# Kernel tuning notes

Hardware: AMD Instinct MI355X
Metric: run time of the kernel (lower is better)

The kernel has to match this reference:

```python
import jax, jax.numpy as jnp
import numpy as np

B, N, D, K, L, H, DFF = 2048, 64, 256, 32, 2, 8, 1024
TEMP = 10.0
EPS = 1e-10


def _ln(x, g, b):
    m = jnp.mean(x, -1, keepdims=True)
    v = jnp.mean((x - m) ** 2, -1, keepdims=True)
    return (x - m) * jax.lax.rsqrt(v + 1e-5) * g + b


def _mha(x, Wqkv, bqkv, Wo, bo):
    b, n, d = x.shape
    dh = d // H
    qkv = x @ Wqkv.T + bqkv                      # [b,n,3d]
    q, k, v = jnp.split(qkv, 3, axis=-1)
    q = q.reshape(b, n, H, dh)
    k = k.reshape(b, n, H, dh)
    v = v.reshape(b, n, H, dh)
    att = jnp.einsum('bqhd,bkhd->bhqk', q, k) / np.float32(np.sqrt(dh))
    att = jax.nn.softmax(att, axis=-1)
    o = jnp.einsum('bhqk,bkhd->bqhd', att, v).reshape(b, n, d)
    return o @ Wo.T + bo


def _encoder(x, Wqkv, bqkv, Wo, bo, ln1_g, ln1_b, ln2_g, ln2_b, W1, b1, W2, b2):
    # torch TransformerEncoder, norm_first=False (post-LN), dropout=0
    for l in range(L):
        x = _ln(x + _mha(x, Wqkv[l], bqkv[l], Wo[l], bo[l]), ln1_g[l], ln1_b[l])
        h = jax.nn.relu(x @ W1[l].T + b1[l]) @ W2[l].T + b2[l]
        x = _ln(x + h, ln2_g[l], ln2_b[l])
    return x


def _cluster_probs_from_emb(emb, mus):
    # ||x - tanh(mu)||^2 via expansion to avoid the [B,N,K,D] intermediate
    mt = jnp.tanh(mus)                                       # [K,D]
    d2 = (jnp.sum(emb ** 2, -1)[..., None]
          - 2.0 * jnp.einsum('bnd,kd->bnk', emb, mt)
          + jnp.sum(mt ** 2, -1))                            # [B,N,K]
    e = jnp.exp(-d2 / TEMP)
    return e / jnp.sum(e, -1, keepdims=True)


def _forward(input_series, init_logits, transition_logits,
             Wqkv, bqkv, Wo, bo, ln1_g, ln1_b, ln2_g, ln2_b,
             W1, b1, W2, b2, mus):
    prob_pi = jax.nn.softmax(init_logits, axis=0)            # [K]
    prob_A = jax.nn.softmax(transition_logits, axis=1)       # [K,K]
    emb_all = _encoder(input_series, Wqkv, bqkv, Wo, bo,
                       ln1_g, ln1_b, ln2_g, ln2_b, W1, b1, W2, b2)
    logits_all = _cluster_probs_from_emb(emb_all, mus)       # [B,N,K]

    log_emit = jnp.log(logits_all + EPS)                     # [B,N,K]
    lt0 = jax.nn.softmax(jnp.log(prob_pi + EPS)[None, :] + log_emit[:, 0], axis=1)

    def step(lt, le):
        lt = jax.nn.softmax(jnp.log(lt @ prob_A + EPS) + le, axis=1)
        return lt, lt

    _, rest = jax.lax.scan(step, lt0, jnp.swapaxes(log_emit[:, 1:], 0, 1))
    cluster_probs = jnp.concatenate([lt0[:, None], jnp.swapaxes(rest, 0, 1)], axis=1)
    entropy_loss = -jnp.mean(jnp.sum(cluster_probs * jnp.log(cluster_probs + EPS), -1))
    return cluster_probs, emb_all, prob_pi, prob_A, entropy_loss


def setup_inputs() -> dict:
    key = jax.random.key(0)
    ks = jax.random.split(key, 10)
    s = jnp.float32(0.02)
    return {
        'input_series': jax.random.normal(ks[0], (B, N, D), jnp.float32),
        'init_logits': jax.random.normal(ks[1], (K,), jnp.float32),
        'transition_logits': jax.random.normal(ks[2], (K, K), jnp.float32),
        'Wqkv': jax.random.normal(ks[3], (L, 3 * D, D), jnp.float32) * s,
        'bqkv': jnp.zeros((L, 3 * D), jnp.float32),
        'Wo': jax.random.normal(ks[4], (L, D, D), jnp.float32) * s,
        'bo': jnp.zeros((L, D), jnp.float32),
        'ln1_g': jnp.ones((L, D), jnp.float32),
        'ln1_b': jnp.zeros((L, D), jnp.float32),
        'ln2_g': jnp.ones((L, D), jnp.float32),
        'ln2_b': jnp.zeros((L, D), jnp.float32),
        'W1': jax.random.normal(ks[5], (L, DFF, D), jnp.float32) * s,
        'b1': jnp.zeros((L, DFF), jnp.float32),
        'W2': jax.random.normal(ks[6], (L, D, DFF), jnp.float32) * s,
        'b2': jnp.zeros((L, D), jnp.float32),
        'mus': jax.random.normal(ks[7], (K, D), jnp.float32),
    }


def reference(input_series, init_logits, transition_logits, Wqkv, bqkv, Wo, bo,
              ln1_g, ln1_b, ln2_g, ln2_b, W1, b1, W2, b2, mus):
    return _forward(input_series, init_logits, transition_logits, Wqkv, bqkv,
                    Wo, bo, ln1_g, ln1_b, ln2_g, ln2_b, W1, b1, W2, b2, mus)
```

## Files before the change

kernel.cpp:

```cpp
#include <hip/hip_runtime.h>

#define BB   2048
#define NNX  64
#define DD   256
#define KKC  32
#define LLN  2
#define HHN  8
#define DHH  32
#define DFFN 1024
#define BNT  (BB*NNX)

typedef short s16x8 __attribute__((ext_vector_type(8)));
typedef float f32x4 __attribute__((ext_vector_type(4)));

#define GLOAD_LDS16(gp, lp) __builtin_amdgcn_global_load_lds( \
    (const __attribute__((address_space(1))) void*)(gp),      \
    (__attribute__((address_space(3))) void*)(lp), 16, 0, 0)

#define WAITVM4() asm volatile("s_waitcnt vmcnt(4)" ::: "memory")
#define WAITVM0() asm volatile("s_waitcnt vmcnt(0)" ::: "memory")
#define WAITLGKM0() do { asm volatile("s_waitcnt lgkmcnt(0)" ::: "memory"); \
                         __builtin_amdgcn_sched_barrier(0); } while (0)
#define SBAR() __builtin_amdgcn_s_barrier()

__device__ __forceinline__ unsigned short f2bf(float f) {
  unsigned int u = __float_as_uint(f);
  u += 0x7fffu + ((u >> 16) & 1u);
  return (unsigned short)(u >> 16);
}
__device__ __forceinline__ float bf2f(unsigned short u) {
  return __uint_as_float(((unsigned int)u) << 16);
}

__global__ __launch_bounds__(256) void cvt_kernel(const float4* __restrict__ src,
                                                  ushort4* __restrict__ dst, int n4) {
  int i = blockIdx.x * 256 + threadIdx.x;
  int st = gridDim.x * 256;
  for (; i < n4; i += st) {
    float4 v = src[i];
    ushort4 o;
    o.x = f2bf(v.x); o.y = f2bf(v.y); o.z = f2bf(v.z); o.w = f2bf(v.w);
    dst[i] = o;
  }
}

__global__ __launch_bounds__(256) void cvtw_kernel(const float4* __restrict__ wq, ushort4* __restrict__ dq,
                                                   const float4* __restrict__ wo, ushort4* __restrict__ dov,
                                                   const float4* __restrict__ w1, ushort4* __restrict__ d1,
                                                   const float4* __restrict__ w2, ushort4* __restrict__ d2) {
  const int n0 = 98304, n1 = 32768, n2 = 131072, n3 = 131072;
  int i = blockIdx.x * 256 + threadIdx.x;
  int st = gridDim.x * 256;
  for (; i < n0 + n1 + n2 + n3; i += st) {
    const float4* s; ushort4* d; int j = i;
    if (j < n0) { s = wq; d = dq; }
    else if ((j -= n0) < n1) { s = wo; d = dov; }
    else if ((j -= n1) < n2) { s = w1; d = d1; }
    else { j -= n2; s = w2; d = d2; }
    float4 v = s[j];
    ushort4 o;
    o.x = f2bf(v.x); o.y = f2bf(v.y); o.z = f2bf(v.z); o.w = f2bf(v.w);
    d[j] = o;
  }
}

__global__ void mt_kernel(const float* __restrict__ mus, float* __restrict__ mtT,
                          float* __restrict__ mtn) {
  int k = threadIdx.x;
  if (k < 32) {
    float acc = 0.f;
    for (int d = 0; d < 256; d++) {
      float t = tanhf(mus[k * 256 + d]);
      mtT[d * 32 + k] = t;
      acc += t * t;
    }
    mtn[k] = acc;
  }
}

__global__ void piA_kernel(const float* __restrict__ il, const float* __restrict__ tl,
                           float* __restrict__ d_pi, float* __restrict__ d_A,
                           float* __restrict__ d_ent) {
  int lane = threadIdx.x;
  if (lane == 0) *d_ent = 0.f;
  if (lane < 32) {
    float v = il[lane];
    float mx = v;
    #pragma unroll
    for (int off = 16; off; off >>= 1) mx = fmaxf(mx, __shfl_xor(mx, off, 32));
    float e = expf(v - mx), sm = e;
    #pragma unroll
    for (int off = 16; off; off >>= 1) sm += __shfl_xor(sm, off, 32);
    d_pi[lane] = e / sm;
    for (int r = 0; r < 32; r++) {
      float a = tl[r * 32 + lane];
      float m2 = a;
      #pragma unroll
      for (int off = 16; off; off >>= 1) m2 = fmaxf(m2, __shfl_xor(m2, off, 32));
      float e2 = expf(a - m2), s2 = e2;
      #pragma unroll
      for (int off = 16; off; off >>= 1) s2 += __shfl_xor(s2, off, 32);
      d_A[r * 32 + lane] = e2 / s2;
    }
  }
}

template <int EPI>
__global__ __launch_bounds__(256, 4) void gemm_nt(const unsigned short* __restrict__ A,
                                                  const unsigned short* __restrict__ Bw,
                                                  const float* __restrict__ bias,
                                                  unsigned short* __restrict__ outp,
                                                  int N, int K, int nx) {
  __shared__ unsigned short lds[16384];
  const int t = threadIdx.x;
  const int bid = blockIdx.x, nwg = gridDim.x;
  const int wg = (bid & 7) * (nwg >> 3) + (bid >> 3);
  const int m0 = (wg / nx) << 7;
  const int n0 = (wg % nx) << 7;
  const int lane = t & 63, w = t >> 6;
  const int wm = w >> 1, wn = w & 1;
  const int lr = lane & 15, lk = lane >> 4;

  const int r0 = t >> 2, sg = t & 3;
  const int s0 = sg ^ ((r0 >> 1) & 3);
  const int r1 = r0 + 64;
  const int s1 = sg ^ ((r1 >> 1) & 3);
  const int aoff0 = (m0 + r0) * K + s0 * 8;
  const int aoff1 = (m0 + r1) * K + s1 * 8;
  const int boff0 = (n0 + r0) * K + s0 * 8;
  const int boff1 = (n0 + r1) * K + s1 * 8;

#define STAGE(buf, k0) do {                                    \
    char* la = (char*)lds + (buf) * 16384;                     \
    GLOAD_LDS16(A + aoff0 + (k0), la + t * 16);                \
    GLOAD_LDS16(A + aoff1 + (k0), la + 4096 + t * 16);         \
    GLOAD_LDS16(Bw + boff0 + (k0), la + 8192 + t * 16);        \
    GLOAD_LDS16(Bw + boff1 + (k0), la + 12288 + t * 16);       \
  } while (0)

  f32x4 acc[4][4];
  #pragma unroll
  for (int i = 0; i < 4; i++)
    #pragma unroll
    for (int j = 0; j < 4; j++) acc[i][j] = (f32x4)(0.f);

  const int ra = wm * 64 + lr, rb = wn * 64 + lr;
  const int sla = lk ^ ((ra >> 1) & 3), slb = lk ^ ((rb >> 1) & 3);

  const int NT = K >> 5;
  STAGE(0, 0);
  STAGE(1, 32);
  WAITVM4();
  SBAR();

  int c = 0;
  for (int kt = 0; kt < NT; kt++) {
    s16x8 af[4], bf[4];
    {
      const unsigned short* ua = lds + c * 8192;
      const unsigned short* ub = ua + 4096;
      #pragma unroll
      for (int mf = 0; mf < 4; mf++)
        af[mf] = *(const s16x8*)&ua[(ra + mf * 16) * 32 + sla * 8];
      #pragma unroll
      for (int nf = 0; nf < 4; nf++)
        bf[nf] = *(const s16x8*)&ub[(rb + nf * 16) * 32 + slb * 8];
    }
    __builtin_amdgcn_s_setprio(1);
    #pragma unroll
    for (int mf = 0; mf < 4; mf++)
      #pragma unroll
      for (int nf = 0; nf < 4; nf++)
        acc[mf][nf] = __builtin_amdgcn_mfma_f32_16x16x32_bf16(af[mf], bf[nf], acc[mf][nf], 0, 0, 0);
    __builtin_amdgcn_s_setprio(0);
    SBAR();
    if (kt < NT - 2) {
      STAGE(c, (kt + 2) << 5);
      WAITVM4();
    } else if (kt == NT - 2) {
      WAITVM0();
    }
    SBAR();
    c ^= 1;
  }
#undef STAGE

  #pragma unroll
  for (int nf = 0; nf < 4; nf++) {
    int col = n0 + wn * 64 + nf * 16 + lr;
    float bv = bias[col];
    #pragma unroll
    for (int mf = 0; mf < 4; mf++)
      #pragma unroll
      for (int r = 0; r < 4; r++) {
        int row = m0 + wm * 64 + mf * 16 + lk * 4 + r;
        float v = acc[mf][nf][r] + bv;
        if (EPI == 1) v = fmaxf(v, 0.f);
        outp[(size_t)row * N + col] = f2bf(v);
      }
  }
}

template <bool WR32>
__global__ __launch_bounds__(512) void gemm_ln(const unsigned short* __restrict__ A,
                                               const unsigned short* __restrict__ Bw,
                                               const float* __restrict__ bias,
                                               const unsigned short* __restrict__ res,
                                               const float* __restrict__ g,
                                               const float* __restrict__ bta,
                                               unsigned short* __restrict__ xb,
                                               float* __restrict__ x32,
                                               int K) {
  __shared__ unsigned short As[128 * 64];
  __shared__ unsigned short Bs[256 * 64];
  __shared__ float stats[2][128][4];
  const int t = threadIdx.x;
  const int nwg = gridDim.x;
  const int bid = blockIdx.x;
  const int wg = (bid & 7) * (nwg >> 3) + (bid >> 3);
  const int m0 = wg << 7;

  const int lane = t & 63, w = t >> 6;
  const int wm = w >> 2, wn = w & 3;
  const int lr = lane & 15, lk = lane >> 4;

  size_t aoff[2], boff[4];
  #pragma unroll
  for (int p = 0; p < 2; p++) {
    int u = p * 512 + t;
    int row = u >> 3, sp = u & 7;
    int seg = sp ^ (((row >> 2) & 1) << 1);
    aoff[p] = (size_t)(m0 + row) * K + seg * 8;
  }
  #pragma unroll
  for (int p = 0; p < 4; p++) {
    int u = p * 512 + t;
    int row = u >> 3, sp = u & 7;
    int seg = sp ^ (((row >> 2) & 1) << 1);
    boff[p] = (size_t)row * K + seg * 8;
  }

  f32x4 acc[4][4];
  #pragma unroll
  for (int i = 0; i < 4; i++)
    #pragma unroll
    for (int j = 0; j < 4; j++) acc[i][j] = (f32x4)(0.f);

  for (int k0 = 0; k0 < K; k0 += 64) {
    #pragma unroll
    for (int p = 0; p < 2; p++)
      GLOAD_LDS16(A + aoff[p] + k0, (char*)As + (p * 512 + t) * 16);
    #pragma unroll
    for (int p = 0; p < 4; p++)
      GLOAD_LDS16(Bw + boff[p] + k0, (char*)Bs + (p * 512 + t) * 16);
    __syncthreads();
    #pragma unroll
    for (int z = 0; z < 2; z++) {
      s16x8 af[4], bfr[4];
      #pragma unroll
      for (int mf = 0; mf < 4; mf++) {
        int row = wm * 64 + mf * 16 + lr;
        int cc = (z * 4 + lk) ^ (((row >> 2) & 1) << 1);
        af[mf] = *(const s16x8*)&As[row * 64 + cc * 8];
      }
      #pragma unroll
      for (int nf = 0; nf < 4; nf++) {
        int row = wn * 64 + nf * 16 + lr;
        int cc = (z * 4 + lk) ^ (((row >> 2) & 1) << 1);
        bfr[nf] = *(const s16x8*)&Bs[row * 64 + cc * 8];
      }
      #pragma unroll
      for (int mf = 0; mf < 4; mf++)
        #pragma unroll
        for (int nf = 0; nf < 4; nf++)
          acc[mf][nf] = __builtin_amdgcn_mfma_f32_16x16x32_bf16(af[mf], bfr[nf], acc[mf][nf], 0, 0, 0);
    }
    __syncthreads();
  }

  float bv[4];
  #pragma unroll
  for (int nf = 0; nf < 4; nf++) bv[nf] = bias[wn * 64 + nf * 16 + lr];

  #pragma unroll
  for (int mf = 0; mf < 4; mf++) {
    #pragma unroll
    for (int r = 0; r < 4; r++) {
      int grow = m0 + wm * 64 + mf * 16 + lk * 4 + r;
      float s = 0.f, q = 0.f;
      #pragma unroll
      for (int nf = 0; nf < 4; nf++) {
        int col = wn * 64 + nf * 16 + lr;
        float v = acc[mf][nf][r] + bv[nf] + bf2f(res[(size_t)grow * 256 + col]);
        acc[mf][nf][r] = v;
        s += v; q += v * v;
      }
      #pragma unroll
      for (int off = 1; off < 16; off <<= 1) { s += __shfl_xor(s, off); q += __shfl_xor(q, off); }
      if (lr == 0) {
        int lrow = wm * 64 + mf * 16 + lk * 4 + r;
        stats[0][lrow][wn] = s;
        stats[1][lrow][wn] = q;
      }
    }
  }
  __syncthreads();

  float gv[4], bbv[4];
  #pragma unroll
  for (int nf = 0; nf < 4; nf++) {
    int col = wn * 64 + nf * 16 + lr;
    gv[nf] = g[col]; bbv[nf] = bta[col];
  }
  #pragma unroll
  for (int mf = 0; mf < 4; mf++) {
    #pragma unroll
    for (int r = 0; r < 4; r++) {
      int lrow = wm * 64 + mf * 16 + lk * 4 + r;
      int grow = m0 + lrow;
      float s4 = stats[0][lrow][0] + stats[0][lrow][1] + stats[0][lrow][2] + stats[0][lrow][3];
      float q4 = stats[1][lrow][0] + stats[1][lrow][1] + stats[1][lrow][2] + stats[1][lrow][3];
      float mean = s4 * (1.f / 256.f);
      float var = q4 * (1.f / 256.f) - mean * mean;
      float rs = rsqrtf(var + 1e-5f);
      #pragma unroll
      for (int nf = 0; nf < 4; nf++) {
        int col = wn * 64 + nf * 16 + lr;
        float val = (acc[mf][nf][r] - mean) * rs * gv[nf] + bbv[nf];
        xb[(size_t)grow * 256 + col] = f2bf(val);
        if (WR32) x32[(size_t)grow * 256 + col] = val;
      }
    }
  }
}

__global__ __launch_bounds__(64) void attn_kernel(const unsigned short* __restrict__ qkv,
                                                  unsigned short* __restrict__ ob) {
  __shared__ unsigned short al[6784];
  unsigned short* qs = al;
  unsigned short* ks = al + 2048;
  unsigned short* vs = al + 4608;
  unsigned short* vt = al;
  unsigned short* ps = al + 2176;
  const int bh = blockIdx.x;
  const int b = bh >> 3, h = bh & 7;
  const int lane = threadIdx.x;
  const int lr = lane & 15, lk = lane >> 4;

  #pragma unroll
  for (int p = 0; p < 4; p++) {
    int u = lane + p * 64;
    int row = u >> 2, seg = u & 3;
    size_t gb = (size_t)(b * 64 + row) * 768 + h * 32 + seg * 8;
    GLOAD_LDS16(qkv + gb, (char*)al + u * 16);
    GLOAD_LDS16(qkv + gb + 256, (char*)al + 4096 + u * 16);
    GLOAD_LDS16(qkv + gb + 512, (char*)al + 9216 + u * 16);
  }
  __syncthreads();

  s16x8 aq[4], bk[4], vchunk[4];
  #pragma unroll
  for (int mi = 0; mi < 4; mi++) aq[mi] = *(const s16x8*)&qs[(mi * 16 + lr) * 32 + lk * 8];
  #pragma unroll
  for (int nj = 0; nj < 4; nj++) bk[nj] = *(const s16x8*)&ks[(nj * 16 + lr) * 32 + lk * 8];
  const int vrow = lane >> 2, vcs = (lane & 3) * 8;
  #pragma unroll
  for (int q = 0; q < 4; q++)
    vchunk[q] = *(const s16x8*)&vs[(q * 16 + vrow) * 32 + vcs];
  WAITLGKM0();

  #pragma unroll
  for (int q = 0; q < 4; q++)
    #pragma unroll
    for (int j = 0; j < 8; j++)
      vt[(vcs + j) * 68 + q * 16 + vrow] = (unsigned short)vchunk[q][j];

  f32x4 s[4][4];
  #pragma unroll
  for (int i = 0; i < 4; i++)
    #pragma unroll
    for (int j = 0; j < 4; j++) s[i][j] = (f32x4)(0.f);
  #pragma unroll
  for (int mi = 0; mi < 4; mi++)
    #pragma unroll
    for (int nj = 0; nj < 4; nj++)
      s[mi][nj] = __builtin_amdgcn_mfma_f32_16x16x32_bf16(aq[mi], bk[nj], s[mi][nj], 0, 0, 0);

  const float scale = 0.17677669529663687f;
  #pragma unroll
  for (int mi = 0; mi < 4; mi++) {
    #pragma unroll
    for (int r = 0; r < 4; r++) {
      float t0 = s[mi][0][r] * scale, t1 = s[mi][1][r] * scale;
      float t2 = s[mi][2][r] * scale, t3 = s[mi][3][r] * scale;
      float mx = fmaxf(fmaxf(t0, t1), fmaxf(t2, t3));
      #pragma unroll
      for (int off = 8; off; off >>= 1) mx = fmaxf(mx, __shfl_xor(mx, off, 16));
      float e0 = expf(t0 - mx), e1 = expf(t1 - mx), e2 = expf(t2 - mx), e3 = expf(t3 - mx);
      float sm = e0 + e1 + e2 + e3;
      #pragma unroll
      for (int off = 8; off; off >>= 1) sm += __shfl_xor(sm, off, 16);
      float inv = 1.f / sm;
      int prow = mi * 16 + lk * 4 + r;
      ps[prow * 72 + lr + 0]  = f2bf(e0 * inv);
      ps[prow * 72 + lr + 16] = f2bf(e1 * inv);
      ps[prow * 72 + lr + 32] = f2bf(e2 * inv);
      ps[prow * 72 + lr + 48] = f2bf(e3 * inv);
    }
  }
  WAITLGKM0();

  f32x4 oacc[4][2];
  #pragma unroll
  for (int i = 0; i < 4; i++) { oacc[i][0] = (f32x4)(0.f); oacc[i][1] = (f32x4)(0.f); }
  #pragma unroll
  for (int kk = 0; kk < 2; kk++) {
    s16x8 bv[2];
    #pragma unroll
    for (int nf = 0; nf < 2; nf++)
      bv[nf] = *(const s16x8*)&vt[(nf * 16 + lr) * 68 + kk * 32 + lk * 8];
    #pragma unroll
    for (int mi = 0; mi < 4; mi++) {
      s16x8 ap = *(const s16x8*)&ps[(mi * 16 + lr) * 72 + kk * 32 + lk * 8];
      #pragma unroll
      for (int nf = 0; nf < 2; nf++)
        oacc[mi][nf] = __builtin_amdgcn_mfma_f32_16x16x32_bf16(ap, bv[nf], oacc[mi][nf], 0, 0, 0);
    }
  }
  #pragma unroll
  for (int mi = 0; mi < 4; mi++)
    #pragma unroll
    for (int nf = 0; nf < 2; nf++)
      #pragma unroll
      for (int r = 0; r < 4; r++) {
        int tok = mi * 16 + lk * 4 + r;
        int c = nf * 16 + lr;
        ob[(size_t)(b * 64 + tok) * 256 + h * 32 + c] = f2bf(oacc[mi][nf][r]);
      }
}

__global__ __launch_bounds__(256) void cluster_kernel(const unsigned short* __restrict__ xb,
                                                      const float* __restrict__ mtT,
                                                      const float* __restrict__ mtn,
                                                      float* __restrict__ log_emit) {
  __shared__ float mts[8192];
  __shared__ float es[4][256];
  const int t = threadIdx.x;
  #pragma unroll
  for (int i = 0; i < 8; i++)
    ((float4*)mts)[i * 256 + t] = ((const float4*)mtT)[i * 256 + t];
  const int w = t >> 6, lane = t & 63;
  const int k = lane & 31, half = lane >> 5;
  const float mtnr = mtn[k];
  __syncthreads();
  #pragma unroll 1
  for (int it = 0; it < 8; it++) {
    size_t tok = (size_t)blockIdx.x * 32 + (size_t)w * 8 + it;
    ushort4 u = *((const ushort4*)(xb + tok * 256) + lane);
    float v0 = bf2f(u.x), v1 = bf2f(u.y), v2 = bf2f(u.z), v3 = bf2f(u.w);
    float4 fv = {v0, v1, v2, v3};
    *(float4*)&es[w][lane * 4] = fv;
    float e2 = v0 * v0 + v1 * v1 + v2 * v2 + v3 * v3;
    #pragma unroll
    for (int off = 1; off < 64; off <<= 1) e2 += __shfl_xor(e2, off);
    float acc = 0.f;
    const float* ep = &es[w][half * 128];
    const float* mp = &mts[half * 128 * 32 + k];
    #pragma unroll
    for (int d = 0; d < 128; d += 4) {
      float4 ev = *(const float4*)(ep + d);
      acc += ev.x * mp[(d + 0) * 32] + ev.y * mp[(d + 1) * 32]
           + ev.z * mp[(d + 2) * 32] + ev.w * mp[(d + 3) * 32];
    }
    acc += __shfl_xor(acc, 32);
    float d2 = e2 - 2.f * acc + mtnr;
    float e = expf(-d2 * 0.1f);
    float sm = e;
    #pragma unroll
    for (int off = 16; off; off >>= 1) sm += __shfl_xor(sm, off, 32);
    if (half == 0) log_emit[tok * 32 + k] = logf(e / sm + 1e-10f);
  }
}

__global__ __launch_bounds__(256) void scan_kernel(const float* __restrict__ log_emit,
                                                   const float* __restrict__ pi,
                                                   const float* __restrict__ A,
                                                   float* __restrict__ cp,
                                                   float* __restrict__ ent) {
  const int g = threadIdx.x >> 5, j = threadIdx.x & 31;
  const int batch = blockIdx.x * 8 + g;
  float regA[32];
  #pragma unroll
  for (int i = 0; i < 32; i++) regA[i] = A[i * 32 + j];
  const float* le = log_emit + (size_t)batch * 64 * 32;
  float* cpo = cp + (size_t)batch * 64 * 32;

  float u = logf(pi[j] + 1e-10f) + le[j];
  float mx = u;
  #pragma unroll
  for (int off = 16; off; off >>= 1) mx = fmaxf(mx, __shfl_xor(mx, off, 32));
  float e = expf(u - mx), sm = e;
  #pragma unroll
  for (int off = 16; off; off >>= 1) sm += __shfl_xor(sm, off, 32);
  float p = e / sm;
  cpo[j] = p;
  float enta = p * logf(p + 1e-10f);

  for (int n = 1; n < 64; n++) {
    float tt = 0.f;
    #pragma unroll
    for (int i = 0; i < 32; i++) tt += __shfl(p, i, 32) * regA[i];
    u = logf(tt + 1e-10f) + le[n * 32 + j];
    mx = u;
    #pragma unroll
    for (int off = 16; off; off >>= 1) mx = fmaxf(mx, __shfl_xor(mx, off, 32));
    e = expf(u - mx); sm = e;
    #pragma unroll
    for (int off = 16; off; off >>= 1) sm += __shfl_xor(sm, off, 32);
    p = e / sm;
    cpo[n * 32 + j] = p;
    enta += p * logf(p + 1e-10f);
  }
  #pragma unroll
  for (int off = 16; off; off >>= 1) enta += __shfl_xor(enta, off, 32);
  if (j == 0) atomicAdd(ent, -enta * (1.f / (2048.f * 64.f)));
}

extern "C" void kernel_launch(void* const* d_in, const int* in_sizes, int n_in,
                              void* d_out, int out_size, void* d_ws, size_t ws_size,
                              hipStream_t stream) {
  const float* input = (const float*)d_in[0];
  const float* init_logits = (const float*)d_in[1];
  const float* trans = (const float*)d_in[2];
  const float* Wqkv = (const float*)d_in[3];
  const float* bqkv = (const float*)d_in[4];
  const float* Wo = (const float*)d_in[5];
  const float* bo = (const float*)d_in[6];
  const float* ln1g = (const float*)d_in[7];
  const float* ln1b = (const float*)d_in[8];
  const float* ln2g = (const float*)d_in[9];
  const float* ln2b = (const float*)d_in[10];
  const float* W1 = (const float*)d_in[11];
  const float* b1 = (const float*)d_in[12];
  const float* W2 = (const float*)d_in[13];
  const float* b2 = (const float*)d_in[14];
  const float* mus = (const float*)d_in[15];

  float* out = (float*)d_out;
  float* cp = out;
  float* x = out + 4194304;
  float* d_pi = out + 37748736;
  float* d_A = out + 37748768;
  float* d_ent = out + 37749792;

  char* ws = (char*)d_ws;
  unsigned short* qkv = (unsigned short*)ws;
  unsigned short* hb = (unsigned short*)ws;
  float* log_emit = (float*)ws;
  unsigned short* ob = (unsigned short*)(ws + 268435456ull);
  unsigned short* xb = (unsigned short*)(ws + 335544320ull);
  unsigned short* wq_b = (unsigned short*)(ws + 402653184ull);
  unsigned short* wo_b = (unsigned short*)(ws + 402653184ull + 786432ull);
  unsigned short* w1_b = (unsigned short*)(ws + 402653184ull + 1048576ull);
  unsigned short* w2_b = (unsigned short*)(ws + 402653184ull + 2097152ull);
  float* mtT = (float*)(ws + 402653184ull + 3145728ull);
  float* mtn = (float*)(ws + 402653184ull + 3178496ull);

  cvt_kernel<<<2048, 256, 0, stream>>>((const float4*)input, (ushort4*)xb, BNT * 256 / 4);
  cvtw_kernel<<<512, 256, 0, stream>>>((const float4*)Wqkv, (ushort4*)wq_b,
                                       (const float4*)Wo, (ushort4*)wo_b,
                                       (const float4*)W1, (ushort4*)w1_b,
                                       (const float4*)W2, (ushort4*)w2_b);
  mt_kernel<<<1, 64, 0, stream>>>(mus, mtT, mtn);
  piA_kernel<<<1, 64, 0, stream>>>(init_logits, trans, d_pi, d_A, d_ent);

  for (int l = 0; l < 2; l++) {
    gemm_nt<0><<<6144, 256, 0, stream>>>(xb, wq_b + l * 196608, bqkv + l * 768,
                                         qkv, 768, 256, 6);
    attn_kernel<<<16384, 64, 0, stream>>>(qkv, ob);
    gemm_ln<false><<<1024, 512, 0, stream>>>(ob, wo_b + l * 65536, bo + l * 256,
                                             xb, ln1g + l * 256, ln1b + l * 256,
                                             xb, nullptr, 256);
    gemm_nt<1><<<8192, 256, 0, stream>>>(xb, w1_b + l * 262144, b1 + l * 1024,
                                         hb, 1024, 256, 8);
    if (l == LLN - 1)
      gemm_ln<true><<<1024, 512, 0, stream>>>(hb, w2_b + l * 262144, b2 + l * 256,
                                              xb, ln2g + l * 256, ln2b + l * 256,
                                              xb, x, 1024);
    else
      gemm_ln<false><<<1024, 512, 0, stream>>>(hb, w2_b + l * 262144, b2 + l * 256,
                                               xb, ln2g + l * 256, ln2b + l * 256,
                                               xb, nullptr, 1024);
  }

  cluster_kernel<<<4096, 256, 0, stream>>>(xb, mtT, mtn, log_emit);
  scan_kernel<<<256, 256, 0, stream>>>(log_emit, d_pi, d_A, cp, d_ent);
}
```

Before: 1.192 ms.

## Compute cluster distances with bf16 MFMA and drop per-token norm term

The cluster kernel is rewritten to compute token-centroid dot products with bf16 16x16x32 MFMA instructions, loading the tanh(mu) matrix as padded bf16 rows in shared memory instead of a transposed fp32 layout. The ||x||^2 term is dropped because it cancels in the softmax over clusters, and a max-subtracted softmax is used instead. Each block now handles 256 tokens with fewer blocks launched. This replaces scalar FMA loops and cross-lane reductions, at the cost of bf16 precision for the centroids.

```diff
diff --git a/kernel.cpp b/kernel.cpp
--- a/kernel.cpp
+++ b/kernel.cpp
@@ -64,14 +64,14 @@
   }
 }
 
-__global__ void mt_kernel(const float* __restrict__ mus, float* __restrict__ mtT,
+__global__ void mt_kernel(const float* __restrict__ mus, unsigned short* __restrict__ mtb,
                           float* __restrict__ mtn) {
   int k = threadIdx.x;
   if (k < 32) {
     float acc = 0.f;
     for (int d = 0; d < 256; d++) {
       float t = tanhf(mus[k * 256 + d]);
-      mtT[d * 32 + k] = t;
+      mtb[k * 264 + d] = f2bf(t);
       acc += t * t;
     }
     mtn[k] = acc;
@@ -440,45 +440,53 @@
 }
 
 __global__ __launch_bounds__(256) void cluster_kernel(const unsigned short* __restrict__ xb,
-                                                      const float* __restrict__ mtT,
+                                                      const unsigned short* __restrict__ mtb,
                                                       const float* __restrict__ mtn,
                                                       float* __restrict__ log_emit) {
-  __shared__ float mts[8192];
-  __shared__ float es[4][256];
+  __shared__ unsigned short ms[32 * 264];
   const int t = threadIdx.x;
-  #pragma unroll
-  for (int i = 0; i < 8; i++)
-    ((float4*)mts)[i * 256 + t] = ((const float4*)mtT)[i * 256 + t];
-  const int w = t >> 6, lane = t & 63;
-  const int k = lane & 31, half = lane >> 5;
-  const float mtnr = mtn[k];
+  for (int i = t; i < 2112; i += 256)
+    ((uint2*)ms)[i] = ((const uint2*)mtb)[i];
+  const int lane = t & 63, w = t >> 6;
+  const int lr = lane & 15, lk = lane >> 4;
+  const float mtn0 = mtn[lr], mtn1 = mtn[16 + lr];
   __syncthreads();
-  #pragma unroll 1
-  for (int it = 0; it < 8; it++) {
-    size_t tok = (size_t)blockIdx.x * 32 + (size_t)w * 8 + it;
-    ushort4 u = *((const ushort4*)(xb + tok * 256) + lane);
-    float v0 = bf2f(u.x), v1 = bf2f(u.y), v2 = bf2f(u.z), v3 = bf2f(u.w);
-    float4 fv = {v0, v1, v2, v3};
-    *(float4*)&es[w][lane * 4] = fv;
-    float e2 = v0 * v0 + v1 * v1 + v2 * v2 + v3 * v3;
-    #pragma unroll
-    for (int off = 1; off < 64; off <<= 1) e2 += __shfl_xor(e2, off);
-    float acc = 0.f;
-    const float* ep = &es[w][half * 128];
-    const float* mp = &mts[half * 128 * 32 + k];
-    #pragma unroll
-    for (int d = 0; d < 128; d += 4) {
-      float4 ev = *(const float4*)(ep + d);
-      acc += ev.x * mp[(d + 0) * 32] + ev.y * mp[(d + 1) * 32]
-           + ev.z * mp[(d + 2) * 32] + ev.w * mp[(d + 3) * 32];
-    }
-    acc += __shfl_xor(acc, 32);
-    float d2 = e2 - 2.f * acc + mtnr;
-    float e = expf(-d2 * 0.1f);
-    float sm = e;
-    #pragma unroll
-    for (int off = 16; off; off >>= 1) sm += __shfl_xor(sm, off, 32);
-    if (half == 0) log_emit[tok * 32 + k] = logf(e / sm + 1e-10f);
+
+  const size_t tok0 = (size_t)blockIdx.x * 256 + (size_t)w * 64;
+  f32x4 s[4][2];
+  #pragma unroll
+  for (int i = 0; i < 4; i++) { s[i][0] = (f32x4)(0.f); s[i][1] = (f32x4)(0.f); }
+
+  #pragma unroll
+  for (int kk = 0; kk < 8; kk++) {
+    s16x8 bf0 = *(const s16x8*)&ms[lr * 264 + lk * 8 + kk * 32];
+    s16x8 bf1 = *(const s16x8*)&ms[(16 + lr) * 264 + lk * 8 + kk * 32];
+    #pragma unroll
+    for (int mi = 0; mi < 4; mi++) {
+      s16x8 af = *(const s16x8*)&xb[(tok0 + mi * 16 + lr) * 256 + lk * 8 + kk * 32];
+      s[mi][0] = __builtin_amdgcn_mfma_f32_16x16x32_bf16(af, bf0, s[mi][0], 0, 0, 0);
+      s[mi][1] = __builtin_amdgcn_mfma_f32_16x16x32_bf16(af, bf1, s[mi][1], 0, 0, 0);
+    }
+  }
+
+  #pragma unroll
+  for (int mi = 0; mi < 4; mi++) {
+    #pragma unroll
+    for (int r = 0; r < 4; r++) {
+      float l0 = (2.f * s[mi][0][r] - mtn0) * 0.1f;
+      float l1 = (2.f * s[mi][1][r] - mtn1) * 0.1f;
+      float mx = fmaxf(l0, l1);
+      #pragma unroll
+      for (int off = 8; off; off >>= 1) mx = fmaxf(mx, __shfl_xor(mx, off, 16));
+      float e0 = expf(l0 - mx), e1 = expf(l1 - mx);
+      float sm = e0 + e1;
+      #pragma unroll
+      for (int off = 8; off; off >>= 1) sm += __shfl_xor(sm, off, 16);
+      float inv = 1.f / sm;
+      size_t row = tok0 + mi * 16 + lk * 4 + r;
+      log_emit[row * 32 + lr]      = logf(e0 * inv + 1e-10f);
+      log_emit[row * 32 + 16 + lr] = logf(e1 * inv + 1e-10f);
+    }
   }
 }
 
@@ -563,7 +571,7 @@
   unsigned short* wo_b = (unsigned short*)(ws + 402653184ull + 786432ull);
   unsigned short* w1_b = (unsigned short*)(ws + 402653184ull + 1048576ull);
   unsigned short* w2_b = (unsigned short*)(ws + 402653184ull + 2097152ull);
-  float* mtT = (float*)(ws + 402653184ull + 3145728ull);
+  unsigned short* mtb = (unsigned short*)(ws + 402653184ull + 3145728ull);
   float* mtn = (float*)(ws + 402653184ull + 3178496ull);
 
   cvt_kernel<<<2048, 256, 0, stream>>>((const float4*)input, (ushort4*)xb, BNT * 256 / 4);
@@ -571,7 +579,7 @@
                                        (const float4*)Wo, (ushort4*)wo_b,
                                        (const float4*)W1, (ushort4*)w1_b,
                                        (const float4*)W2, (ushort4*)w2_b);
-  mt_kernel<<<1, 64, 0, stream>>>(mus, mtT, mtn);
+  mt_kernel<<<1, 64, 0, stream>>>(mus, mtb, mtn);
   piA_kernel<<<1, 64, 0, stream>>>(init_logits, trans, d_pi, d_A, d_ent);
 
   for (int l = 0; l < 2; l++) {
@@ -593,6 +601,6 @@
                                                xb, nullptr, 1024);
   }
 
-  cluster_kernel<<<4096, 256, 0, stream>>>(xb, mtT, mtn, log_emit);
+  cluster_kernel<<<512, 256, 0, stream>>>(xb, mtb, mtn, log_emit);
   scan_kernel<<<256, 256, 0, stream>>>(log_emit, d_pi, d_A, cp, d_ent);
 }
```

Measured after the change: 1.141 ms. 1.04x faster.
